# Optimization experiments

Hardware: AMD Instinct MI355X
Metric: run time of the kernel (lower is better)

## Reference

```python
import jax, jax.numpy as jnp
import numpy as np

B, L, H, NE, SPAN = 16, 2048, 768, 64, 4
EPS_COS = 1e-8   # torch cosine_similarity eps
EPS_STD = 1e-5   # std stabilizer from the module


def _linear_init(key, fan_in, fan_out):
    s = 1.0 / np.sqrt(fan_in)
    kw, kb = jax.random.split(key)
    w = jax.random.uniform(kw, (fan_in, fan_out), jnp.float32, -s, s)
    b = jax.random.uniform(kb, (fan_out,), jnp.float32, -s, s)
    return w, b


def setup_inputs() -> dict:
    key = jax.random.key(0)
    ks = jax.random.split(key, 6)
    w1, b1 = _linear_init(ks[0], 2 * H + 1, H)
    w2, b2 = _linear_init(ks[1], H, 512)
    w3, b3 = _linear_init(ks[2], 512, 256)
    w4, b4 = _linear_init(ks[3], 256, 2)
    x = jax.random.normal(ks[4], (B, L, H), jnp.float32)
    entity_starts = jax.random.randint(ks[5], (B, NE), 0, L - SPAN)
    threshold = jnp.float32(0.9)
    return dict(x=x, threshold=threshold,
                w1=w1, b1=b1, w2=w2, b2=b2, w3=w3, b3=b3, w4=w4, b4=b4,
                entity_starts=entity_starts)


def reference(x, threshold, w1, b1, w2, b2, w3, b3, w4, b4, entity_starts):
    # --- per-entity span max-pool (segment-max over x) ---
    # gather span tokens: [B, NE*SPAN] token indices into the L axis
    idx = (entity_starts[:, :, None] + jnp.arange(SPAN)).reshape(B, NE * SPAN)
    spans = jnp.take_along_axis(x, idx[:, :, None], axis=1)      # [B, NE*SPAN, H]
    emb = spans.reshape(B, NE, SPAN, H).max(axis=2)               # [B, NE, H]

    # --- pairwise cosine similarity per batch ---
    norm = jnp.maximum(jnp.linalg.norm(emb, axis=-1, keepdims=True), EPS_COS)
    n = emb / norm
    cos = jnp.einsum('bie,bje->bij', n, n)                        # [B, NE, NE]
    std = jnp.std(cos, axis=(1, 2), ddof=1, keepdims=True)        # torch .std() is unbiased
    sim = (cos - threshold) / (std + EPS_STD)
    sim = jnp.triu(sim, k=1)

    # --- all i<j pairs: [sim, emb_i, emb_j] ---
    iu, ju = np.triu_indices(NE, k=1)                             # static pair indices
    feats = jnp.concatenate(
        [sim[:, iu, ju, None], emb[:, iu, :], emb[:, ju, :]], axis=-1
    ).reshape(-1, 2 * H + 1)                                      # [B*P, 2H+1]

    # --- classifier MLP (dropout = identity at eval) ---
    h = jax.nn.relu(feats @ w1 + b1)
    h = jax.nn.relu(h @ w2 + b2)
    h = jax.nn.relu(h @ w3 + b3)
    logits = h @ w4 + b4                                          # [B*P, 2]
    return logits
```

## Files before the change

kernel.cpp:

```cpp
#include <hip/hip_runtime.h>
#include <cstdint>
#include <cstddef>

#define B_    16
#define L_    2048
#define H_    768
#define NE_   64
#define SPAN_ 4
#define NPAIR 2016
#define NROWS (B_ * NPAIR)

typedef __bf16 bf16_t;
typedef __bf16 bf16x8 __attribute__((ext_vector_type(8)));
typedef __bf16 bf16x4 __attribute__((ext_vector_type(4)));
typedef float  floatx4 __attribute__((ext_vector_type(4)));

#define AS1 __attribute__((address_space(1)))
#define AS3 __attribute__((address_space(3)))

#define OFF_EMBH   ((size_t)3145728)
#define OFF_SIM    ((size_t)8126464)
#define OFF_W1ABT  ((size_t)8255488)
#define OFF_W2T    ((size_t)10614784)
#define OFF_W3T    ((size_t)11401216)
#define OFF_C1     ((size_t)11663360)
#define OFF_H2     ((size_t)67500032)
#define OFF_FLAG   ((size_t)117045248)
#define OFF_CANON  ((size_t)117045504)

#define SWZ(colb, row) ((colb) ^ (((row) & 3) << 4))

__device__ inline bf16_t cvt_elem(const void* p, size_t i, int isf) {
  if (isf) return (bf16_t)(((const float*)p)[i]);
  return ((const bf16_t*)p)[i];
}

__global__ __launch_bounds__(1024) void prep_embsim_kernel(
    const unsigned short* __restrict__ xu,
    const void* __restrict__ xv, const int* __restrict__ starts,
    const void* __restrict__ thr_ptr,
    const void* __restrict__ w1, const void* __restrict__ w2,
    const void* __restrict__ w3, const void* __restrict__ b1,
    const void* __restrict__ b2, const void* __restrict__ b3,
    const void* __restrict__ w4, const void* __restrict__ b4,
    int* __restrict__ flagout,
    bf16_t* __restrict__ w1abT, bf16_t* __restrict__ w2T,
    bf16_t* __restrict__ w3T, bf16_t* __restrict__ canon,
    bf16_t* __restrict__ embh, float* __restrict__ simv) {
  __shared__ __align__(16) char shbuf[98304];
  __shared__ int   tot[16];
  __shared__ float red1[16], red2[16];
  __shared__ float scale_s, thr_s;

  int blk = blockIdx.x;
  int t = threadIdx.x;

  {
    int bad = 0;
    for (int i = t; i < 4096; i += 1024) {
      int e = (xu[i] >> 7) & 0xFF;
      if (e > 133 || (e > 0 && e < 90)) bad++;
    }
    for (int off = 32; off > 0; off >>= 1) bad += __shfl_down(bad, off, 64);
    if ((t & 63) == 0) tot[t >> 6] = bad;
    __syncthreads();
  }
  int sumb = 0;
#pragma unroll
  for (int i = 0; i < 16; i++) sumb += tot[i];
  int isf = (sumb > 200) ? 1 : 0;
  __syncthreads();

  if (blk < 16) {
    bf16_t* nrm = (bf16_t*)shbuf;
    int b = blk;
    int e   = t >> 4;
    int l16 = t & 15;
    int d0  = l16 * 48;
    int st  = starts[b * NE_ + e];
    size_t off = ((size_t)(b * L_ + st)) * H_;
    float ss = 0.f;
    bf16x8 pv[6];
    if (isf) {
      const float* xp = (const float*)xv + off + d0;
#pragma unroll
      for (int c8 = 0; c8 < 6; c8++) {
        const float* p = xp + c8 * 8;
        bf16x8 o;
#pragma unroll
        for (int h = 0; h < 2; h++) {
          floatx4 r0 = *(const floatx4*)(p + h * 4);
          floatx4 r1 = *(const floatx4*)(p + H_ + h * 4);
          floatx4 r2 = *(const floatx4*)(p + 2 * H_ + h * 4);
          floatx4 r3 = *(const floatx4*)(p + 3 * H_ + h * 4);
#pragma unroll
          for (int q = 0; q < 4; q++) {
            float v = fmaxf(fmaxf(r0[q], r1[q]), fmaxf(r2[q], r3[q]));
            ss += v * v;
            o[h * 4 + q] = (bf16_t)v;
          }
        }
        pv[c8] = o;
      }
    } else {
      const bf16_t* xp = (const bf16_t*)xv + off + d0;
#pragma unroll
      for (int c8 = 0; c8 < 6; c8++) {
        const bf16_t* p = xp + c8 * 8;
        bf16x8 r0 = *(const bf16x8*)(p);
        bf16x8 r1 = *(const bf16x8*)(p + H_);
        bf16x8 r2 = *(const bf16x8*)(p + 2 * H_);
        bf16x8 r3 = *(const bf16x8*)(p + 3 * H_);
        bf16x8 o;
#pragma unroll
        for (int q = 0; q < 8; q++) {
          float v = fmaxf(fmaxf((float)r0[q], (float)r1[q]),
                          fmaxf((float)r2[q], (float)r3[q]));
          ss += v * v;
          o[q] = (bf16_t)v;
        }
        pv[c8] = o;
      }
    }
#pragma unroll
    for (int d = 1; d < 16; d <<= 1) ss += __shfl_xor(ss, d, 64);
    float inv = 1.0f / fmaxf(sqrtf(ss), 1e-8f);

    size_t gb = ((size_t)(b * 64 + e)) * 768 + d0;
    int rowbyte = e * 1536;
    int xw = (e & 7) << 4;
#pragma unroll
    for (int c8 = 0; c8 < 6; c8++) {
      *(bf16x8*)(embh + gb + c8 * 8) = pv[c8];
      bf16x8 o;
#pragma unroll
      for (int q = 0; q < 8; q++) o[q] = (bf16_t)((float)pv[c8][q] * inv);
      int byo = (rowbyte + (d0 + c8 * 8) * 2) ^ xw;
      *(bf16x8*)((char*)nrm + byo) = o;
    }
    __syncthreads();

    int w = t >> 6, lane = t & 63;
    int quad = lane >> 4, l15 = lane & 15;
    int ti = w >> 2, tj = w & 3;
    int rowA = ti * 16 + l15, rowB = tj * 16 + l15;
    int xa = (rowA & 7) << 4, xb = (rowB & 7) << 4;
    const char* nb = (const char*)nrm;
    floatx4 acc = {};
#pragma unroll 4
    for (int k0 = 0; k0 < 768; k0 += 32) {
      int cb = (k0 + quad * 8) * 2;
      bf16x8 aF = *(const bf16x8*)(nb + ((rowA * 1536 + cb) ^ xa));
      bf16x8 bF = *(const bf16x8*)(nb + ((rowB * 1536 + cb) ^ xb));
      acc = __builtin_amdgcn_mfma_f32_16x16x32_bf16(aF, bF, acc, 0, 0, 0);
    }

    float s1 = acc[0] + acc[1] + acc[2] + acc[3];
    float s2 = acc[0] * acc[0] + acc[1] * acc[1] + acc[2] * acc[2] + acc[3] * acc[3];
#pragma unroll
    for (int d = 32; d > 0; d >>= 1) {
      s1 += __shfl_xor(s1, d, 64);
      s2 += __shfl_xor(s2, d, 64);
    }
    if (lane == 0) { red1[w] = s1; red2[w] = s2; }
    __syncthreads();
    if (t == 0) {
      float S1 = 0.f, S2 = 0.f;
#pragma unroll
      for (int i = 0; i < 16; i++) { S1 += red1[i]; S2 += red2[i]; }
      float mean = S1 * (1.0f / 4096.0f);
      float var = (S2 - 4096.0f * mean * mean) * (1.0f / 4095.0f);
      float sd = sqrtf(fmaxf(var, 0.f));
      scale_s = 1.0f / (sd + 1e-5f);
      thr_s = isf ? *(const float*)thr_ptr : (float)(*(const bf16_t*)thr_ptr);
    }
    __syncthreads();
    float sc = scale_s, th = thr_s;
    int ibase = ti * 16 + quad * 4;
    int j = tj * 16 + l15;
#pragma unroll
    for (int r = 0; r < 4; r++) {
      int i = ibase + r;
      if (j > i) {
        int p = i * 63 - (i * (i - 1)) / 2 + (j - i - 1);
        simv[b * NPAIR + p] = (acc[r] - th) * sc;
      }
    }
    return;
  }

  for (int u = blk - 16; u < 417; u += 240) {
    if (u == 0) {
      if (t == 0) flagout[0] = isf;
      for (int idx = t; idx < 2818; idx += 1024) {
        if (idx < 768)       canon[idx] = cvt_elem(w1, idx, isf);
        else if (idx < 1536) canon[idx] = cvt_elem(b1, idx - 768, isf);
        else if (idx < 2048) canon[idx] = cvt_elem(b2, idx - 1536, isf);
        else if (idx < 2304) canon[idx] = cvt_elem(b3, idx - 2048, isf);
        else if (idx < 2816) canon[idx] = cvt_elem(w4, idx - 2304, isf);
        else                 canon[idx] = cvt_elem(b4, idx - 2816, isf);
      }
    } else {
      int tix = u - 1;
      const void* src; size_t srcoff; bf16_t* dst; int K, N;
      if (tix < 144)      { src = w1; srcoff = 768;               dst = w1abT;          K = 768; N = 768; }
      else if (tix < 288) { src = w1; srcoff = (size_t)769 * 768; dst = w1abT + 589824; K = 768; N = 768; tix -= 144; }
      else if (tix < 384) { src = w2; srcoff = 0;                 dst = w2T;            K = 768; N = 512; tix -= 288; }
      else                { src = w3; srcoff = 0;                 dst = w3T;            K = 512; N = 256; tix -= 384; }
      int tiles_k = K >> 6;
      int tn_t = tix / tiles_k, tk_t = tix - tn_t * tiles_k;
      bf16_t (*tile)[65] = (bf16_t(*)[65])shbuf;
      int ty = t >> 6, tx = t & 63;
      __syncthreads();
#pragma unroll
      for (int p = 0; p < 4; p++) {
        int kk = tk_t * 64 + p * 16 + ty;
        int nn = tn_t * 64 + tx;
        tile[p * 16 + ty][tx] = cvt_elem(src, srcoff + (size_t)kk * N + nn, isf);
      }
      __syncthreads();
#pragma unroll
      for (int p = 0; p < 4; p++) {
        int nn = tn_t * 64 + p * 16 + ty;
        int kk = tk_t * 64 + tx;
        dst[(size_t)nn * K + kk] = tile[tx][p * 16 + ty];
      }
    }
  }
}

__global__ __launch_bounds__(256) void gemm1_kernel(
    const bf16_t* __restrict__ A, const bf16_t* __restrict__ Bt,
    float* __restrict__ C) {
  const int K = 768, N = 1536;
  __shared__ __align__(16) bf16_t Asm[64 * 32];
  __shared__ __align__(16) bf16_t Bsm[128 * 32];
  int bm = blockIdx.x, bn = blockIdx.y;
  int t = threadIdx.x;
  int w = t >> 6, lane = t & 63;
  int quad = lane >> 4, l15 = lane & 15;
  int wm = w >> 1, wn = w & 1;

  floatx4 acc[2][4] = {};
  const char* Abase = (const char*)(A + (size_t)bm * 64 * K);
  const char* Bbase = (const char*)(Bt + (size_t)bn * 128 * K);
  const int rowbytes = K * 2;

  for (int k0 = 0; k0 < K; k0 += 32) {
    {
      int fo = w * 1024 + lane * 16;
      int row = fo >> 6, colb = fo & 63;
      __builtin_amdgcn_global_load_lds(
          (AS1 char*)(Abase + (size_t)row * rowbytes + k0 * 2 + SWZ(colb, row)),
          (AS3 char*)((char*)Asm + w * 1024),
          16, 0, 0);
    }
#pragma unroll
    for (int it = 0; it < 2; it++) {
      int fo = (w * 2 + it) * 1024 + lane * 16;
      int row = fo >> 6, colb = fo & 63;
      __builtin_amdgcn_global_load_lds(
          (AS1 char*)(Bbase + (size_t)row * rowbytes + k0 * 2 + SWZ(colb, row)),
          (AS3 char*)((char*)Bsm + (w * 2 + it) * 1024),
          16, 0, 0);
    }
    __syncthreads();

    bf16x8 aF[2], bF[4];
#pragma unroll
    for (int tm = 0; tm < 2; tm++) {
      int ra = wm * 32 + tm * 16 + l15;
      aF[tm] = *((const bf16x8*)((const char*)Asm + ra * 64 + SWZ(quad * 16, ra)));
    }
#pragma unroll
    for (int tn = 0; tn < 4; tn++) {
      int rb = wn * 64 + tn * 16 + l15;
      bF[tn] = *((const bf16x8*)((const char*)Bsm + rb * 64 + SWZ(quad * 16, rb)));
    }
#pragma unroll
    for (int tm = 0; tm < 2; tm++)
#pragma unroll
      for (int tn = 0; tn < 4; tn++)
        acc[tm][tn] = __builtin_amdgcn_mfma_f32_16x16x32_bf16(aF[tm], bF[tn], acc[tm][tn], 0, 0, 0);
    __syncthreads();
  }

#pragma unroll
  for (int tm = 0; tm < 2; tm++) {
    int grow0 = bm * 64 + wm * 32 + tm * 16 + quad * 4;
#pragma unroll
    for (int tn = 0; tn < 4; tn++) {
      int gcol = bn * 128 + wn * 64 + tn * 16 + l15;
#pragma unroll
      for (int r = 0; r < 4; r++)
        C[(size_t)(grow0 + r) * N + gcol] = acc[tm][tn][r];
    }
  }
}

__global__ __launch_bounds__(512, 4) void gemm2_fused_kernel(
    const float* __restrict__ C1, const float* __restrict__ sim,
    const bf16_t* __restrict__ w2T, const bf16_t* __restrict__ canon,
    bf16_t* __restrict__ h2) {
  __shared__ __align__(16) bf16_t Asm[2][128 * 40];
  __shared__ __align__(16) bf16_t Bsm[2][256 * 32];
  __shared__ int   rowI[128], rowJ[128];
  __shared__ float rowS[128];
  __shared__ bf16_t w1s[768], b1s[768];
  __shared__ float b2s[256];
  int bm = blockIdx.x, bn = blockIdx.y;
  int t = threadIdx.x;

  if (t < 128) {
    int r = bm * 128 + t;
    int b = r / NPAIR, p = r - b * NPAIR;
    int i = 0, rem = p;
    while (rem >= 63 - i) { rem -= 63 - i; i++; }
    rowI[t] = b * 64 + i;
    rowJ[t] = b * 64 + i + 1 + rem;
    rowS[t] = sim[r];
  }
  for (int c = t; c < 768; c += 512) { w1s[c] = canon[c]; b1s[c] = canon[768 + c]; }
  if (t < 256) b2s[t] = (float)canon[1536 + bn * 256 + t];
  __syncthreads();

  int w = t >> 6, lane = t & 63;
  int quad = lane >> 4, l15 = lane & 15;
  int wm = w >> 2, wn = w & 3;
  floatx4 acc[4][4] = {};

  const char* Bbase = (const char*)(w2T + (size_t)bn * 256 * 768);

  int arow = t >> 2;
  int acolc = (t & 3) * 8;
  const float* Ai = C1 + (size_t)rowI[arow] * 1536 + acolc;
  const float* Aj = C1 + (size_t)rowJ[arow] * 1536 + 768 + acolc;
  float s = rowS[arow];

  float4 pi0 = *(const float4*)(Ai);
  float4 pi1 = *(const float4*)(Ai + 4);
  float4 pj0 = *(const float4*)(Aj);
  float4 pj1 = *(const float4*)(Aj + 4);
#pragma unroll
  for (int it = 0; it < 2; it++) {
    int fo = w * 2048 + it * 1024 + lane * 16;
    int row = fo >> 6, colb = fo & 63;
    __builtin_amdgcn_global_load_lds(
        (AS1 char*)(Bbase + (size_t)row * 1536 + SWZ(colb, row)),
        (AS3 char*)((char*)&Bsm[0][0] + w * 2048 + it * 1024),
        16, 0, 0);
  }
  {
    int kc = acolc;
    bf16x8 o;
    const bf16x8 wv8 = *(const bf16x8*)(w1s + kc);
    const bf16x8 bv8 = *(const bf16x8*)(b1s + kc);
    o[0] = (bf16_t)fmaxf(pi0.x + pj0.x + s * (float)wv8[0] + (float)bv8[0], 0.f);
    o[1] = (bf16_t)fmaxf(pi0.y + pj0.y + s * (float)wv8[1] + (float)bv8[1], 0.f);
    o[2] = (bf16_t)fmaxf(pi0.z + pj0.z + s * (float)wv8[2] + (float)bv8[2], 0.f);
    o[3] = (bf16_t)fmaxf(pi0.w + pj0.w + s * (float)wv8[3] + (float)bv8[3], 0.f);
    o[4] = (bf16_t)fmaxf(pi1.x + pj1.x + s * (float)wv8[4] + (float)bv8[4], 0.f);
    o[5] = (bf16_t)fmaxf(pi1.y + pj1.y + s * (float)wv8[5] + (float)bv8[5], 0.f);
    o[6] = (bf16_t)fmaxf(pi1.z + pj1.z + s * (float)wv8[6] + (float)bv8[6], 0.f);
    o[7] = (bf16_t)fmaxf(pi1.w + pj1.w + s * (float)wv8[7] + (float)bv8[7], 0.f);
    *(bf16x8*)(&Asm[0][arow * 40 + acolc]) = o;
  }
  pi0 = *(const float4*)(Ai + 32);
  pi1 = *(const float4*)(Ai + 36);
  pj0 = *(const float4*)(Aj + 32);
  pj1 = *(const float4*)(Aj + 36);
  __syncthreads();

  for (int kt = 0; kt < 24; ++kt) {
    int cur = kt & 1, nxt = cur ^ 1;
    if (kt < 23) {
      int k1 = (kt + 1) * 32;
#pragma unroll
      for (int it = 0; it < 2; it++) {
        int fo = w * 2048 + it * 1024 + lane * 16;
        int row = fo >> 6, colb = fo & 63;
        __builtin_amdgcn_global_load_lds(
            (AS1 char*)(Bbase + (size_t)row * 1536 + k1 * 2 + SWZ(colb, row)),
            (AS3 char*)((char*)&Bsm[nxt][0] + w * 2048 + it * 1024),
            16, 0, 0);
      }
      {
        int kc = k1 + acolc;
        bf16x8 o;
        const bf16x8 wv8 = *(const bf16x8*)(w1s + kc);
        const bf16x8 bv8 = *(const bf16x8*)(b1s + kc);
        o[0] = (bf16_t)fmaxf(pi0.x + pj0.x + s * (float)wv8[0] + (float)bv8[0], 0.f);
        o[1] = (bf16_t)fmaxf(pi0.y + pj0.y + s * (float)wv8[1] + (float)bv8[1], 0.f);
        o[2] = (bf16_t)fmaxf(pi0.z + pj0.z + s * (float)wv8[2] + (float)bv8[2], 0.f);
        o[3] = (bf16_t)fmaxf(pi0.w + pj0.w + s * (float)wv8[3] + (float)bv8[3], 0.f);
        o[4] = (bf16_t)fmaxf(pi1.x + pj1.x + s * (float)wv8[4] + (float)bv8[4], 0.f);
        o[5] = (bf16_t)fmaxf(pi1.y + pj1.y + s * (float)wv8[5] + (float)bv8[5], 0.f);
        o[6] = (bf16_t)fmaxf(pi1.z + pj1.z + s * (float)wv8[6] + (float)bv8[6], 0.f);
        o[7] = (bf16_t)fmaxf(pi1.w + pj1.w + s * (float)wv8[7] + (float)bv8[7], 0.f);
        *(bf16x8*)(&Asm[nxt][arow * 40 + acolc]) = o;
      }
      if (kt < 22) {
        int k2 = (kt + 2) * 32;
        pi0 = *(const float4*)(Ai + k2);
        pi1 = *(const float4*)(Ai + k2 + 4);
        pj0 = *(const float4*)(Aj + k2);
        pj1 = *(const float4*)(Aj + k2 + 4);
      }
    }

    bf16x8 aF[4], bF[4];
#pragma unroll
    for (int tm = 0; tm < 4; tm++)
      aF[tm] = *((const bf16x8*)(&Asm[cur][(wm * 64 + tm * 16 + l15) * 40 + quad * 8]));
#pragma unroll
    for (int tn = 0; tn < 4; tn++) {
      int rb = wn * 64 + tn * 16 + l15;
      bF[tn] = *((const bf16x8*)((const char*)&Bsm[cur][0] + rb * 64 + SWZ(quad * 16, rb)));
    }
#pragma unroll
    for (int tm = 0; tm < 4; tm++)
#pragma unroll
      for (int tn = 0; tn < 4; tn++)
        acc[tm][tn] = __builtin_amdgcn_mfma_f32_16x16x32_bf16(aF[tm], bF[tn], acc[tm][tn], 0, 0, 0);
    __syncthreads();
  }

#pragma unroll
  for (int tm = 0; tm < 4; tm++) {
    int grow0 = bm * 128 + wm * 64 + tm * 16 + quad * 4;
#pragma unroll
    for (int tn = 0; tn < 4; tn++) {
      int lcol = wn * 64 + tn * 16 + l15;
      int gcol = bn * 256 + lcol;
#pragma unroll
      for (int r = 0; r < 4; r++) {
        float v = fmaxf(acc[tm][tn][r] + b2s[lcol], 0.f);
        h2[(size_t)(grow0 + r) * 512 + gcol] = (bf16_t)v;
      }
    }
  }
}

__global__ __launch_bounds__(256) void gemm3_fused_kernel(
    const bf16_t* __restrict__ h2, const bf16_t* __restrict__ w3T,
    const bf16_t* __restrict__ canon, const int* __restrict__ flagp,
    void* __restrict__ out) {
  __shared__ __align__(16) bf16_t Asm[2][64 * 32];
  __shared__ __align__(16) bf16_t Bsm[2][256 * 32];
  __shared__ float part[64][2][4];
  __shared__ float w4s[512];
  __shared__ float b3s[256];
  int bm = blockIdx.x;
  int t = threadIdx.x;
  int w = t >> 6, lane = t & 63;
  int quad = lane >> 4, l15 = lane & 15;

  w4s[t]       = (float)canon[2304 + t];
  w4s[256 + t] = (float)canon[2304 + 256 + t];
  b3s[t]       = (float)canon[2048 + t];

  floatx4 acc[4][4] = {};
  const char* Abase = (const char*)(h2 + (size_t)bm * 64 * 512);
  const char* Bbase = (const char*)w3T;

  {
    int fo = w * 1024 + lane * 16;
    int row = fo >> 6, colb = fo & 63;
    __builtin_amdgcn_global_load_lds(
        (AS1 char*)(Abase + (size_t)row * 1024 + SWZ(colb, row)),
        (AS3 char*)((char*)&Asm[0][0] + w * 1024),
        16, 0, 0);
  }
#pragma unroll
  for (int it = 0; it < 4; it++) {
    int fo = w * 4096 + it * 1024 + lane * 16;
    int row = fo >> 6, colb = fo & 63;
    __builtin_amdgcn_global_load_lds(
        (AS1 char*)(Bbase + (size_t)row * 1024 + SWZ(colb, row)),
        (AS3 char*)((char*)&Bsm[0][0] + w * 4096 + it * 1024),
        16, 0, 0);
  }
  __syncthreads();

  for (int kt = 0; kt < 16; ++kt) {
    int cur = kt & 1, nxt = cur ^ 1;
    if (kt < 15) {
      int k1 = (kt + 1) * 32;
      {
        int fo = w * 1024 + lane * 16;
        int row = fo >> 6, colb = fo & 63;
        __builtin_amdgcn_global_load_lds(
            (AS1 char*)(Abase + (size_t)row * 1024 + k1 * 2 + SWZ(colb, row)),
            (AS3 char*)((char*)&Asm[nxt][0] + w * 1024),
            16, 0, 0);
      }
#pragma unroll
      for (int it = 0; it < 4; it++) {
        int fo = w * 4096 + it * 1024 + lane * 16;
        int row = fo >> 6, colb = fo & 63;
        __builtin_amdgcn_global_load_lds(
            (AS1 char*)(Bbase + (size_t)row * 1024 + k1 * 2 + SWZ(colb, row)),
            (AS3 char*)((char*)&Bsm[nxt][0] + w * 4096 + it * 1024),
            16, 0, 0);
      }
    }

    bf16x8 aF[4], bF[4];
#pragma unroll
    for (int tm = 0; tm < 4; tm++) {
      int ra = tm * 16 + l15;
      aF[tm] = *((const bf16x8*)((const char*)&Asm[cur][0] + ra * 64 + SWZ(quad * 16, ra)));
    }
#pragma unroll
    for (int tn = 0; tn < 4; tn++) {
      int rb = w * 64 + tn * 16 + l15;
      bF[tn] = *((const bf16x8*)((const char*)&Bsm[cur][0] + rb * 64 + SWZ(quad * 16, rb)));
    }
#pragma unroll
    for (int tm = 0; tm < 4; tm++)
#pragma unroll
      for (int tn = 0; tn < 4; tn++)
        acc[tm][tn] = __builtin_amdgcn_mfma_f32_16x16x32_bf16(aF[tm], bF[tn], acc[tm][tn], 0, 0, 0);
    __syncthreads();
  }

#pragma unroll
  for (int tm = 0; tm < 4; tm++) {
#pragma unroll
    for (int reg = 0; reg < 4; reg++) {
      float p0 = 0.f, p1 = 0.f;
#pragma unroll
      for (int tn = 0; tn < 4; tn++) {
        int col = w * 64 + tn * 16 + l15;
        float v = fmaxf(acc[tm][tn][reg] + b3s[col], 0.f);
        p0 += v * w4s[col * 2];
        p1 += v * w4s[col * 2 + 1];
      }
#pragma unroll
      for (int d = 1; d < 16; d <<= 1) {
        p0 += __shfl_xor(p0, d, 64);
        p1 += __shfl_xor(p1, d, 64);
      }
      if (l15 == 0) {
        int r = tm * 16 + quad * 4 + reg;
        part[r][0][w] = p0;
        part[r][1][w] = p1;
      }
    }
  }
  __syncthreads();
  if (t < 128) {
    int r = t >> 1, c = t & 1;
    float v = part[r][c][0] + part[r][c][1] + part[r][c][2] + part[r][c][3]
            + (float)canon[2816 + c];
    size_t rg = (size_t)bm * 64 + r;
    if (flagp[0]) ((float*)out)[rg * 2 + c] = v;
    else          ((bf16_t*)out)[rg * 2 + c] = (bf16_t)v;
  }
}

extern "C" void kernel_launch(void* const* d_in, const int* in_sizes, int n_in,
                              void* d_out, int out_size, void* d_ws, size_t ws_size,
                              hipStream_t stream) {
  const void* x      = d_in[0];
  const void* thr    = d_in[1];
  const void* w1     = d_in[2];
  const void* b1     = d_in[3];
  const void* w2     = d_in[4];
  const void* b2     = d_in[5];
  const void* w3     = d_in[6];
  const void* b3     = d_in[7];
  const void* w4     = d_in[8];
  const void* b4     = d_in[9];
  const int*  starts = (const int*)d_in[10];

  char* ws = (char*)d_ws;
  bf16_t* embh  = (bf16_t*)(ws + OFF_EMBH);
  float*  simv  = (float*)(ws + OFF_SIM);
  bf16_t* w1abT = (bf16_t*)(ws + OFF_W1ABT);
  bf16_t* w2T   = (bf16_t*)(ws + OFF_W2T);
  bf16_t* w3T   = (bf16_t*)(ws + OFF_W3T);
  float*  C1    = (float*)(ws + OFF_C1);
  bf16_t* h2    = (bf16_t*)(ws + OFF_H2);
  int*    flag  = (int*)(ws + OFF_FLAG);
  bf16_t* canon = (bf16_t*)(ws + OFF_CANON);

  prep_embsim_kernel<<<256, 1024, 0, stream>>>(
      (const unsigned short*)x, x, starts, thr,
      w1, w2, w3, b1, b2, b3, w4, b4,
      flag, w1abT, w2T, w3T, canon, embh, simv);

  {
    dim3 g(1024 / 64, 1536 / 128);
    gemm1_kernel<<<g, 256, 0, stream>>>(embh, w1abT, C1);
  }

  {
    dim3 g(NROWS / 128, 2);
    gemm2_fused_kernel<<<g, 512, 0, stream>>>(C1, simv, w2T, canon, h2);
  }

  gemm3_fused_kernel<<<NROWS / 64, 256, 0, stream>>>(h2, w3T, canon, flag, d_out);
}
```

Baseline: 263.9 us.

## Split span pooling across blocks and fuse cosine stats into double-buffered GEMM1

Span max-pooling is spread over 64 blocks of 16 entities each, instead of 16 blocks holding 64 entities, and the normalized embeddings are written to a global buffer. The cosine-similarity and std computation moves out of the prep kernel into a combined kernel that also runs GEMM1, whose K loop is now double-buffered in LDS. The aim is to shorten the critical path of the prep kernel and hide global-to-LDS latency in GEMM1. The cost is an extra global round-trip for the normalized embeddings, and the 16 cosine blocks share the GEMM1 launch, so they may become stragglers.

```diff
diff --git a/kernel.cpp b/kernel.cpp
--- a/kernel.cpp
+++ b/kernel.cpp
@@ -19,6 +19,7 @@
 #define AS3 __attribute__((address_space(3)))
 
 #define OFF_EMBH   ((size_t)3145728)
+#define OFF_NRMG   ((size_t)4718592)
 #define OFF_SIM    ((size_t)8126464)
 #define OFF_W1ABT  ((size_t)8255488)
 #define OFF_W2T    ((size_t)10614784)
@@ -35,10 +36,9 @@
   return ((const bf16_t*)p)[i];
 }
 
-__global__ __launch_bounds__(1024) void prep_embsim_kernel(
+__global__ __launch_bounds__(1024) void prep_kernel(
     const unsigned short* __restrict__ xu,
     const void* __restrict__ xv, const int* __restrict__ starts,
-    const void* __restrict__ thr_ptr,
     const void* __restrict__ w1, const void* __restrict__ w2,
     const void* __restrict__ w3, const void* __restrict__ b1,
     const void* __restrict__ b2, const void* __restrict__ b3,
@@ -46,12 +46,9 @@
     int* __restrict__ flagout,
     bf16_t* __restrict__ w1abT, bf16_t* __restrict__ w2T,
     bf16_t* __restrict__ w3T, bf16_t* __restrict__ canon,
-    bf16_t* __restrict__ embh, float* __restrict__ simv) {
-  __shared__ __align__(16) char shbuf[98304];
-  __shared__ int   tot[16];
-  __shared__ float red1[16], red2[16];
-  __shared__ float scale_s, thr_s;
-
+    bf16_t* __restrict__ embh, bf16_t* __restrict__ nrm_g) {
+  __shared__ bf16_t tile[64][65];
+  __shared__ int tot[16];
   int blk = blockIdx.x;
   int t = threadIdx.x;
 
@@ -71,126 +68,64 @@
   int isf = (sumb > 200) ? 1 : 0;
   __syncthreads();
 
-  if (blk < 16) {
-    bf16_t* nrm = (bf16_t*)shbuf;
-    int b = blk;
-    int e   = t >> 4;
-    int l16 = t & 15;
-    int d0  = l16 * 48;
-    int st  = starts[b * NE_ + e];
-    size_t off = ((size_t)(b * L_ + st)) * H_;
-    float ss = 0.f;
-    bf16x8 pv[6];
-    if (isf) {
-      const float* xp = (const float*)xv + off + d0;
-#pragma unroll
-      for (int c8 = 0; c8 < 6; c8++) {
-        const float* p = xp + c8 * 8;
-        bf16x8 o;
-#pragma unroll
-        for (int h = 0; h < 2; h++) {
-          floatx4 r0 = *(const floatx4*)(p + h * 4);
-          floatx4 r1 = *(const floatx4*)(p + H_ + h * 4);
-          floatx4 r2 = *(const floatx4*)(p + 2 * H_ + h * 4);
-          floatx4 r3 = *(const floatx4*)(p + 3 * H_ + h * 4);
+  for (int u = blk; u < 481; u += 256) {
+    if (u < 64) {
+      int lane = t & 63;
+      int entity = u * 16 + (t >> 6);
+      int st = starts[entity];
+      int b = entity >> 6;
+      size_t off = ((size_t)(b * L_ + st)) * H_;
+      int d0 = lane * 12;
+      float pool[12];
+      float ss = 0.f;
+      if (isf) {
+        const float* xp = (const float*)xv + off + d0;
+#pragma unroll
+        for (int k = 0; k < 3; k++) {
+          floatx4 r0 = *(const floatx4*)(xp + k * 4);
+          floatx4 r1 = *(const floatx4*)(xp + H_ + k * 4);
+          floatx4 r2 = *(const floatx4*)(xp + 2 * H_ + k * 4);
+          floatx4 r3 = *(const floatx4*)(xp + 3 * H_ + k * 4);
 #pragma unroll
           for (int q = 0; q < 4; q++) {
             float v = fmaxf(fmaxf(r0[q], r1[q]), fmaxf(r2[q], r3[q]));
+            pool[k * 4 + q] = v;
             ss += v * v;
-            o[h * 4 + q] = (bf16_t)v;
           }
         }
-        pv[c8] = o;
-      }
-    } else {
-      const bf16_t* xp = (const bf16_t*)xv + off + d0;
-#pragma unroll
-      for (int c8 = 0; c8 < 6; c8++) {
-        const bf16_t* p = xp + c8 * 8;
-        bf16x8 r0 = *(const bf16x8*)(p);
-        bf16x8 r1 = *(const bf16x8*)(p + H_);
-        bf16x8 r2 = *(const bf16x8*)(p + 2 * H_);
-        bf16x8 r3 = *(const bf16x8*)(p + 3 * H_);
-        bf16x8 o;
-#pragma unroll
-        for (int q = 0; q < 8; q++) {
-          float v = fmaxf(fmaxf((float)r0[q], (float)r1[q]),
-                          fmaxf((float)r2[q], (float)r3[q]));
-          ss += v * v;
-          o[q] = (bf16_t)v;
+      } else {
+        const bf16_t* xp = (const bf16_t*)xv + off + d0;
+#pragma unroll
+        for (int k = 0; k < 3; k++) {
+          bf16x4 r0 = *(const bf16x4*)(xp + k * 4);
+          bf16x4 r1 = *(const bf16x4*)(xp + H_ + k * 4);
+          bf16x4 r2 = *(const bf16x4*)(xp + 2 * H_ + k * 4);
+          bf16x4 r3 = *(const bf16x4*)(xp + 3 * H_ + k * 4);
+#pragma unroll
+          for (int q = 0; q < 4; q++) {
+            float v = fmaxf(fmaxf((float)r0[q], (float)r1[q]),
+                            fmaxf((float)r2[q], (float)r3[q]));
+            pool[k * 4 + q] = v;
+            ss += v * v;
+          }
         }
-        pv[c8] = o;
-      }
-    }
-#pragma unroll
-    for (int d = 1; d < 16; d <<= 1) ss += __shfl_xor(ss, d, 64);
-    float inv = 1.0f / fmaxf(sqrtf(ss), 1e-8f);
-
-    size_t gb = ((size_t)(b * 64 + e)) * 768 + d0;
-    int rowbyte = e * 1536;
-    int xw = (e & 7) << 4;
-#pragma unroll
-    for (int c8 = 0; c8 < 6; c8++) {
-      *(bf16x8*)(embh + gb + c8 * 8) = pv[c8];
-      bf16x8 o;
-#pragma unroll
-      for (int q = 0; q < 8; q++) o[q] = (bf16_t)((float)pv[c8][q] * inv);
-      int byo = (rowbyte + (d0 + c8 * 8) * 2) ^ xw;
-      *(bf16x8*)((char*)nrm + byo) = o;
-    }
-    __syncthreads();
-
-    int w = t >> 6, lane = t & 63;
-    int quad = lane >> 4, l15 = lane & 15;
-    int ti = w >> 2, tj = w & 3;
-    int rowA = ti * 16 + l15, rowB = tj * 16 + l15;
-    int xa = (rowA & 7) << 4, xb = (rowB & 7) << 4;
-    const char* nb = (const char*)nrm;
-    floatx4 acc = {};
-#pragma unroll 4
-    for (int k0 = 0; k0 < 768; k0 += 32) {
-      int cb = (k0 + quad * 8) * 2;
-      bf16x8 aF = *(const bf16x8*)(nb + ((rowA * 1536 + cb) ^ xa));
-      bf16x8 bF = *(const bf16x8*)(nb + ((rowB * 1536 + cb) ^ xb));
-      acc = __builtin_amdgcn_mfma_f32_16x16x32_bf16(aF, bF, acc, 0, 0, 0);
-    }
-
-    float s1 = acc[0] + acc[1] + acc[2] + acc[3];
-    float s2 = acc[0] * acc[0] + acc[1] * acc[1] + acc[2] * acc[2] + acc[3] * acc[3];
-#pragma unroll
-    for (int d = 32; d > 0; d >>= 1) {
-      s1 += __shfl_xor(s1, d, 64);
-      s2 += __shfl_xor(s2, d, 64);
-    }
-    if (lane == 0) { red1[w] = s1; red2[w] = s2; }
-    __syncthreads();
-    if (t == 0) {
-      float S1 = 0.f, S2 = 0.f;
-#pragma unroll
-      for (int i = 0; i < 16; i++) { S1 += red1[i]; S2 += red2[i]; }
-      float mean = S1 * (1.0f / 4096.0f);
-      float var = (S2 - 4096.0f * mean * mean) * (1.0f / 4095.0f);
-      float sd = sqrtf(fmaxf(var, 0.f));
-      scale_s = 1.0f / (sd + 1e-5f);
-      thr_s = isf ? *(const float*)thr_ptr : (float)(*(const bf16_t*)thr_ptr);
-    }
-    __syncthreads();
-    float sc = scale_s, th = thr_s;
-    int ibase = ti * 16 + quad * 4;
-    int j = tj * 16 + l15;
-#pragma unroll
-    for (int r = 0; r < 4; r++) {
-      int i = ibase + r;
-      if (j > i) {
-        int p = i * 63 - (i * (i - 1)) / 2 + (j - i - 1);
-        simv[b * NPAIR + p] = (acc[r] - th) * sc;
-      }
-    }
-    return;
-  }
-
-  for (int u = blk - 16; u < 417; u += 240) {
-    if (u == 0) {
+      }
+#pragma unroll
+      for (int d = 1; d < 64; d <<= 1) ss += __shfl_xor(ss, d, 64);
+      float inv = 1.0f / fmaxf(sqrtf(ss), 1e-8f);
+      size_t base = (size_t)entity * 768 + d0;
+#pragma unroll
+      for (int k = 0; k < 3; k++) {
+        bf16x4 op, on;
+#pragma unroll
+        for (int q = 0; q < 4; q++) {
+          op[q] = (bf16_t)pool[k * 4 + q];
+          on[q] = (bf16_t)(pool[k * 4 + q] * inv);
+        }
+        *(bf16x4*)(embh + base + k * 4) = op;
+        *(bf16x4*)(nrm_g + base + k * 4) = on;
+      }
+    } else if (u == 64) {
       if (t == 0) flagout[0] = isf;
       for (int idx = t; idx < 2818; idx += 1024) {
         if (idx < 768)       canon[idx] = cvt_elem(w1, idx, isf);
@@ -201,7 +136,7 @@
         else                 canon[idx] = cvt_elem(b4, idx - 2816, isf);
       }
     } else {
-      int tix = u - 1;
+      int tix = u - 65;
       const void* src; size_t srcoff; bf16_t* dst; int K, N;
       if (tix < 144)      { src = w1; srcoff = 768;               dst = w1abT;          K = 768; N = 768; }
       else if (tix < 288) { src = w1; srcoff = (size_t)769 * 768; dst = w1abT + 589824; K = 768; N = 768; tix -= 144; }
@@ -209,7 +144,6 @@
       else                { src = w3; srcoff = 0;                 dst = w3T;            K = 512; N = 256; tix -= 384; }
       int tiles_k = K >> 6;
       int tn_t = tix / tiles_k, tk_t = tix - tn_t * tiles_k;
-      bf16_t (*tile)[65] = (bf16_t(*)[65])shbuf;
       int ty = t >> 6, tx = t & 63;
       __syncthreads();
 #pragma unroll
@@ -229,53 +163,145 @@
   }
 }
 
-__global__ __launch_bounds__(256) void gemm1_kernel(
-    const bf16_t* __restrict__ A, const bf16_t* __restrict__ Bt,
-    float* __restrict__ C) {
-  const int K = 768, N = 1536;
-  __shared__ __align__(16) bf16_t Asm[64 * 32];
-  __shared__ __align__(16) bf16_t Bsm[128 * 32];
-  int bm = blockIdx.x, bn = blockIdx.y;
+__global__ __launch_bounds__(256) void cosgemm1_kernel(
+    const bf16_t* __restrict__ nrm_g, const bf16_t* __restrict__ embh,
+    const bf16_t* __restrict__ w1abT, const int* __restrict__ flagp,
+    const void* __restrict__ thr_ptr, float* __restrict__ simv,
+    float* __restrict__ C1) {
+  __shared__ __align__(16) char shb[98304];
+  __shared__ float red1[4], red2[4];
+  __shared__ float scale_s, thr_s;
+  int blk = blockIdx.x;
   int t = threadIdx.x;
   int w = t >> 6, lane = t & 63;
   int quad = lane >> 4, l15 = lane & 15;
+
+  if (blk < 16) {
+    bf16_t* nrm = (bf16_t*)shb;
+    int b = blk;
+    const bf16_t* src = nrm_g + (size_t)b * 64 * 768;
+    {
+      int lr = t >> 2, c0 = (t & 3) * 192;
+      for (int i = 0; i < 24; i++) {
+        int col = c0 + i * 8;
+        bf16x8 v = *(const bf16x8*)(src + lr * 768 + col);
+        *(bf16x8*)((char*)nrm + ((lr * 1536 + col * 2) ^ ((lr & 7) << 4))) = v;
+      }
+    }
+    __syncthreads();
+
+    int rowA = w * 16 + l15;
+    int xa = (rowA & 7) << 4;
+    floatx4 acc[4] = {};
+    for (int k0 = 0; k0 < 768; k0 += 32) {
+      int cb = (k0 + quad * 8) * 2;
+      bf16x8 aF = *(const bf16x8*)((char*)nrm + ((rowA * 1536 + cb) ^ xa));
+#pragma unroll
+      for (int tj = 0; tj < 4; tj++) {
+        int rb = tj * 16 + l15;
+        bf16x8 bF = *(const bf16x8*)((char*)nrm + ((rb * 1536 + cb) ^ ((rb & 7) << 4)));
+        acc[tj] = __builtin_amdgcn_mfma_f32_16x16x32_bf16(aF, bF, acc[tj], 0, 0, 0);
+      }
+    }
+
+    float s1 = 0.f, s2 = 0.f;
+#pragma unroll
+    for (int tj = 0; tj < 4; tj++)
+#pragma unroll
+      for (int r = 0; r < 4; r++) { s1 += acc[tj][r]; s2 += acc[tj][r] * acc[tj][r]; }
+#pragma unroll
+    for (int d = 1; d < 64; d <<= 1) {
+      s1 += __shfl_xor(s1, d, 64);
+      s2 += __shfl_xor(s2, d, 64);
+    }
+    if (lane == 0) { red1[w] = s1; red2[w] = s2; }
+    __syncthreads();
+    if (t == 0) {
+      float S1 = red1[0] + red1[1] + red1[2] + red1[3];
+      float S2 = red2[0] + red2[1] + red2[2] + red2[3];
+      float mean = S1 * (1.0f / 4096.0f);
+      float var = (S2 - 4096.0f * mean * mean) * (1.0f / 4095.0f);
+      float sd = sqrtf(fmaxf(var, 0.f));
+      scale_s = 1.0f / (sd + 1e-5f);
+      thr_s = flagp[0] ? *(const float*)thr_ptr : (float)(*(const bf16_t*)thr_ptr);
+    }
+    __syncthreads();
+    float sc = scale_s, th = thr_s;
+#pragma unroll
+    for (int tj = 0; tj < 4; tj++) {
+      int j = tj * 16 + l15;
+#pragma unroll
+      for (int r = 0; r < 4; r++) {
+        int i = w * 16 + quad * 4 + r;
+        if (j > i) {
+          int p = i * 63 - (i * (i - 1)) / 2 + (j - i - 1);
+          simv[b * NPAIR + p] = (acc[tj][r] - th) * sc;
+        }
+      }
+    }
+    return;
+  }
+
+  const int K = 768, N = 1536;
+  int bi = blk - 16;
+  int bm = bi / 12, bn = bi - bm * 12;
   int wm = w >> 1, wn = w & 1;
 
   floatx4 acc[2][4] = {};
-  const char* Abase = (const char*)(A + (size_t)bm * 64 * K);
-  const char* Bbase = (const char*)(Bt + (size_t)bn * 128 * K);
+  const char* Abase = (const char*)(embh + (size_t)bm * 64 * K);
+  const char* Bbase = (const char*)(w1abT + (size_t)bn * 128 * K);
   const int rowbytes = K * 2;
 
-  for (int k0 = 0; k0 < K; k0 += 32) {
-    {
-      int fo = w * 1024 + lane * 16;
-      int row = fo >> 6, colb = fo & 63;
-      __builtin_amdgcn_global_load_lds(
-          (AS1 char*)(Abase + (size_t)row * rowbytes + k0 * 2 + SWZ(colb, row)),
-          (AS3 char*)((char*)Asm + w * 1024),
-          16, 0, 0);
-    }
-#pragma unroll
-    for (int it = 0; it < 2; it++) {
-      int fo = (w * 2 + it) * 1024 + lane * 16;
-      int row = fo >> 6, colb = fo & 63;
-      __builtin_amdgcn_global_load_lds(
-          (AS1 char*)(Bbase + (size_t)row * rowbytes + k0 * 2 + SWZ(colb, row)),
-          (AS3 char*)((char*)Bsm + (w * 2 + it) * 1024),
-          16, 0, 0);
-    }
-    __syncthreads();
-
+  {
+    int fo = w * 1024 + lane * 16;
+    int row = fo >> 6, colb = fo & 63;
+    __builtin_amdgcn_global_load_lds(
+        (AS1 char*)(Abase + (size_t)row * rowbytes + SWZ(colb, row)),
+        (AS3 char*)(shb + w * 1024), 16, 0, 0);
+  }
+#pragma unroll
+  for (int it = 0; it < 2; it++) {
+    int fo = (w * 2 + it) * 1024 + lane * 16;
+    int row = fo >> 6, colb = fo & 63;
+    __builtin_amdgcn_global_load_lds(
+        (AS1 char*)(Bbase + (size_t)row * rowbytes + SWZ(colb, row)),
+        (AS3 char*)(shb + 8192 + (w * 2 + it) * 1024), 16, 0, 0);
+  }
+  __syncthreads();
+
+  for (int kt = 0; kt < 24; ++kt) {
+    int cur = kt & 1, nxt = cur ^ 1;
+    if (kt < 23) {
+      int k1 = (kt + 1) * 32;
+      {
+        int fo = w * 1024 + lane * 16;
+        int row = fo >> 6, colb = fo & 63;
+        __builtin_amdgcn_global_load_lds(
+            (AS1 char*)(Abase + (size_t)row * rowbytes + k1 * 2 + SWZ(colb, row)),
+            (AS3 char*)(shb + nxt * 4096 + w * 1024), 16, 0, 0);
+      }
+#pragma unroll
+      for (int it = 0; it < 2; it++) {
+        int fo = (w * 2 + it) * 1024 + lane * 16;
+        int row = fo >> 6, colb = fo & 63;
+        __builtin_amdgcn_global_load_lds(
+            (AS1 char*)(Bbase + (size_t)row * rowbytes + k1 * 2 + SWZ(colb, row)),
+            (AS3 char*)(shb + 8192 + nxt * 8192 + (w * 2 + it) * 1024), 16, 0, 0);
+      }
+    }
+
+    const char* Ac = shb + cur * 4096;
+    const char* Bc = shb + 8192 + cur * 8192;
     bf16x8 aF[2], bF[4];
 #pragma unroll
     for (int tm = 0; tm < 2; tm++) {
       int ra = wm * 32 + tm * 16 + l15;
-      aF[tm] = *((const bf16x8*)((const char*)Asm + ra * 64 + SWZ(quad * 16, ra)));
+      aF[tm] = *((const bf16x8*)(Ac + ra * 64 + SWZ(quad * 16, ra)));
     }
 #pragma unroll
     for (int tn = 0; tn < 4; tn++) {
       int rb = wn * 64 + tn * 16 + l15;
-      bF[tn] = *((const bf16x8*)((const char*)Bsm + rb * 64 + SWZ(quad * 16, rb)));
+      bF[tn] = *((const bf16x8*)(Bc + rb * 64 + SWZ(quad * 16, rb)));
     }
 #pragma unroll
     for (int tm = 0; tm < 2; tm++)
@@ -293,7 +319,7 @@
       int gcol = bn * 128 + wn * 64 + tn * 16 + l15;
 #pragma unroll
       for (int r = 0; r < 4; r++)
-        C[(size_t)(grow0 + r) * N + gcol] = acc[tm][tn][r];
+        C1[(size_t)(grow0 + r) * N + gcol] = acc[tm][tn][r];
     }
   }
 }
@@ -576,6 +602,7 @@
 
   char* ws = (char*)d_ws;
   bf16_t* embh  = (bf16_t*)(ws + OFF_EMBH);
+  bf16_t* nrm_g = (bf16_t*)(ws + OFF_NRMG);
   float*  simv  = (float*)(ws + OFF_SIM);
   bf16_t* w1abT = (bf16_t*)(ws + OFF_W1ABT);
   bf16_t* w2T   = (bf16_t*)(ws + OFF_W2T);
@@ -585,15 +612,13 @@
   int*    flag  = (int*)(ws + OFF_FLAG);
   bf16_t* canon = (bf16_t*)(ws + OFF_CANON);
 
-  prep_embsim_kernel<<<256, 1024, 0, stream>>>(
-      (const unsigned short*)x, x, starts, thr,
+  prep_kernel<<<256, 1024, 0, stream>>>(
+      (const unsigned short*)x, x, starts,
       w1, w2, w3, b1, b2, b3, w4, b4,
-      flag, w1abT, w2T, w3T, canon, embh, simv);
-
-  {
-    dim3 g(1024 / 64, 1536 / 128);
-    gemm1_kernel<<<g, 256, 0, stream>>>(embh, w1abT, C1);
-  }
+      flag, w1abT, w2T, w3T, canon, embh, nrm_g);
+
+  cosgemm1_kernel<<<208, 256, 0, stream>>>(nrm_g, embh, w1abT, flag, thr,
+                                           simv, C1);
 
   {
     dim3 g(NROWS / 128, 2);
```

Result: faster. 229.3 us (-13.1%).
